# Kernel optimization log

Measured on AMD Instinct MI355X. Metric: run time of the kernel, lower is better.

Reference implementation:

```python
import jax, jax.numpy as jnp
import numpy as np

B, T, EMB, HEAD = 8, 4096, 1024, 64  # batch, seq (=block_sz), emb_dim, head_sz


def setup_inputs() -> dict:
    key = jax.random.key(0)
    kx, kw = jax.random.split(key)
    x = jax.random.normal(kx, (B, T, EMB), dtype=jnp.float32)
    W = jax.random.normal(kw, (EMB, 3 * HEAD), dtype=jnp.float32) * 0.02
    return {"x": x, "W": W}


def reference(x, W):
    # fused QKV projection: [B,T,EMB] @ [EMB,3*HEAD] -> [B,T,3*HEAD]
    kqv = x @ W
    k, q, v = jnp.split(kqv, 3, axis=-1)  # source order: k, q, v
    head_sz = q.shape[-1]
    # causal attention scores: [B,T,T]
    scores = jnp.einsum('btd,bsd->bts', q, k) / jnp.sqrt(jnp.float32(head_sz))
    causal_mask = jnp.triu(jnp.full((scores.shape[1], scores.shape[2]), -jnp.inf, dtype=scores.dtype), 1)
    w = jax.nn.softmax(scores + causal_mask, axis=-1)
    # dropout p=0.0 -> identity
    out = jnp.einsum('bts,bsd->btd', w, v)  # [B,T,HEAD]
    return out
```

## Files before the change

kernel.cpp:

```cpp
#include <hip/hip_runtime.h>
#include <hip/hip_bf16.h>

#define BATCH 8
#define SEQ 4096
#define EMB 1024
#define HEAD 64
#define N3 192

#define BM 64
#define BK 64
#define NT (EMB / BK)
#define LSTR 72

typedef __attribute__((ext_vector_type(4))) float f32x4;
typedef __attribute__((ext_vector_type(8))) short bf16x8;
typedef __attribute__((ext_vector_type(4))) short short4v;
typedef __attribute__((ext_vector_type(4))) float float4v;
typedef __attribute__((ext_vector_type(2))) unsigned int u32x2;

#define LOG2E 1.4426950408889634f
#define QSCALE (0.125f * LOG2E)


static __device__ __forceinline__ unsigned short f2bf(float f) {
  unsigned int x = __builtin_bit_cast(unsigned int, f);
  x += 0x7fffu + ((x >> 16) & 1u);
  return (unsigned short)(x >> 16);
}

__global__ __launch_bounds__(256) void wt_kernel(const float* __restrict__ W,
                                                 unsigned short* __restrict__ Wt) {
  int idx = blockIdx.x * 256 + threadIdx.x;
  int k = idx / N3, c = idx % N3;
  Wt[(size_t)c * EMB + k] = f2bf(W[idx]);
}

__global__ __launch_bounds__(256, 2) void qkv_kernel(const float* __restrict__ x,
                                                     const unsigned short* __restrict__ Wt,
                                                     unsigned short* __restrict__ PK,
                                                     unsigned short* __restrict__ PQ,
                                                     unsigned short* __restrict__ PV) {
  __shared__ unsigned short Asm[2][BM][LSTR];
  __shared__ unsigned short Bsm[2][N3][LSTR];

  const int tid = threadIdx.x;
  const int wid = tid >> 6;
  const int lane = tid & 63;
  const int l16 = lane & 15;
  const int lg = lane >> 4;
  const int m0 = blockIdx.x * BM;

  const int ar0 = tid >> 4;
  const int ac4 = tid & 15;
  const int br0 = tid >> 3;
  const int bc = tid & 7;

  const float* xa = x + (size_t)(m0 + ar0) * EMB + ac4 * 4;
  const unsigned short* wb = Wt + (size_t)br0 * EMB + bc * 8;

  f32x4 acc[4][3];
#pragma unroll
  for (int mi = 0; mi < 4; ++mi)
#pragma unroll
    for (int ni = 0; ni < 3; ++ni) acc[mi][ni] = (f32x4)0.0f;

  float4v av[4];
  bf16x8 bv[6];

#define ISSUE_LOADS(K0)                                                        \
  {                                                                            \
    _Pragma("unroll") for (int i = 0; i < 4; ++i)                              \
        av[i] = *(const float4v*)(xa + (size_t)(16 * i) * EMB + (K0));         \
    _Pragma("unroll") for (int i = 0; i < 6; ++i)                              \
        bv[i] = *(const bf16x8*)(wb + (size_t)(32 * i) * EMB + (K0));          \
  }

#define WRITE_LDS(BUF)                                                         \
  {                                                                            \
    _Pragma("unroll") for (int i = 0; i < 4; ++i) {                            \
      short4v p;                                                               \
      _Pragma("unroll") for (int j = 0; j < 4; ++j)                            \
          p[j] = (short)f2bf(av[i][j]);                                        \
      *(short4v*)&Asm[BUF][ar0 + 16 * i][ac4 * 4] = p;                         \
    }                                                                          \
    _Pragma("unroll") for (int i = 0; i < 6; ++i)                              \
        *(bf16x8*)&Bsm[BUF][br0 + 32 * i][bc * 8] = bv[i];                     \
  }

#define COMPUTE(BUF)                                                           \
  {                                                                            \
    _Pragma("unroll") for (int kh = 0; kh < 2; ++kh) {                         \
      bf16x8 af[4], bfr[3];                                                    \
      _Pragma("unroll") for (int mi = 0; mi < 4; ++mi)                         \
          af[mi] = *(const bf16x8*)&Asm[BUF][mi * 16 + l16][kh * 32 + lg * 8]; \
      _Pragma("unroll") for (int ni = 0; ni < 3; ++ni)                         \
          bfr[ni] = *(const bf16x8*)&Bsm[BUF][wid * 48 + ni * 16 + l16][kh * 32 + lg * 8]; \
      _Pragma("unroll") for (int mi = 0; mi < 4; ++mi)                         \
        _Pragma("unroll") for (int ni = 0; ni < 3; ++ni)                       \
            acc[mi][ni] = __builtin_amdgcn_mfma_f32_16x16x32_bf16(             \
                af[mi], bfr[ni], acc[mi][ni], 0, 0, 0);                        \
    }                                                                          \
  }

  ISSUE_LOADS(0)
  WRITE_LDS(0)
  __syncthreads();

  int cur = 0;
  for (int t = 0; t < NT; ++t) {
    if (t < NT - 1) ISSUE_LOADS((t + 1) * BK)
    COMPUTE(cur)
    if (t < NT - 1) {
      WRITE_LDS(cur ^ 1)
    }
    __syncthreads();
    cur ^= 1;
  }
#undef ISSUE_LOADS
#undef WRITE_LDS
#undef COMPUTE

#pragma unroll
  for (int mi = 0; mi < 4; ++mi) {
#pragma unroll
    for (int ni = 0; ni < 3; ++ni) {
      const int n = wid * 48 + ni * 16 + l16;
#pragma unroll
      for (int r = 0; r < 4; ++r) {
        const int row = m0 + mi * 16 + lg * 4 + r;
        const int bb = row >> 12;
        const int ss = row & (SEQ - 1);
        const float v = acc[mi][ni][r];
        if (n < 64) {
          PK[(((size_t)bb * 256 + (ss >> 4)) * 2 + (n >> 5)) * 512 +
             (ss & 15) * 32 + (n & 31)] = f2bf(v);
        } else if (n < 128) {
          const int d = n - 64;
          PQ[(((size_t)bb * 256 + (ss >> 4)) * 2 + (d >> 5)) * 512 +
             (ss & 15) * 32 + (d & 31)] = f2bf(v * QSCALE);
        } else {
          const int d = n - 128;
          PV[(((size_t)bb * 64 + (ss >> 6)) * 8 + (d >> 4) * 2 + ((ss >> 5) & 1)) * 512 +
             (d & 15) * 32 + (ss & 31)] = f2bf(v);
        }
      }
    }
  }
}

__global__ __launch_bounds__(256, 4) void attn_kernel(const unsigned short* __restrict__ PK,
                                                      const unsigned short* __restrict__ PQ,
                                                      const unsigned short* __restrict__ PV,
                                                      float* __restrict__ out) {
  __shared__ float Msm[4][16];
  __shared__ float Lsm[4][16];
  __shared__ float Osm[4][4][16][17];
  __shared__ unsigned short Pl[4][2][16][LSTR];

  const int tid = threadIdx.x;
  const int wid = tid >> 6;
  const int lane = tid & 63;
  const int l16 = lane & 15;
  const int lg = lane >> 4;
  const int lam = (l16 * 4 + lg) * 8;

  const int Bid = blockIdx.x;
  const int b = Bid & 7;
  const int i_ = (Bid >> 3) & 31;
  const int j_ = Bid >> 8;
  const int p = (j_ == 0) ? i_ : (j_ == 1) ? (127 - i_) : (j_ == 2) ? (32 + i_) : (95 - i_);
  const int qc0 = 2 * p, qc1 = 2 * p + 1;
  const int q0a = qc0 * 16, q0b = qc1 * 16;
  const int T_total = (q0b + 16 + 63) >> 6;
  const int t0 = (wid * T_total) >> 2;
  const int t1 = ((wid + 1) * T_total) >> 2;

  const unsigned short* pkb = PK + (size_t)b * 256 * 1024;
  const unsigned short* pqb = PQ + (size_t)b * 256 * 1024;
  const unsigned short* pvb = PV + (size_t)b * 64 * 8 * 512;

  bf16x8 qa0 = *(const bf16x8*)(pqb + ((size_t)qc0 * 2 + 0) * 512 + lam);
  bf16x8 qa1 = *(const bf16x8*)(pqb + ((size_t)qc0 * 2 + 1) * 512 + lam);
  bf16x8 qb0 = *(const bf16x8*)(pqb + ((size_t)qc1 * 2 + 0) * 512 + lam);
  bf16x8 qb1 = *(const bf16x8*)(pqb + ((size_t)qc1 * 2 + 1) * 512 + lam);

  f32x4 oA[4], oB[4];
#pragma unroll
  for (int dd = 0; dd < 4; ++dd) { oA[dd] = (f32x4)0.0f; oB[dd] = (f32x4)0.0f; }
  float mA = -3.0e38f, lA = 0.0f, mB = -3.0e38f, lB = 0.0f;

  for (int it = t0; it < t1; ++it) {
    const int kv0 = it << 6;

    f32x4 s0[4], s1[4];
#pragma unroll
    for (int t = 0; t < 4; ++t) {
      const unsigned short* kp = pkb + ((size_t)(it * 4 + t) * 2) * 512 + lam;
      bf16x8 kfa = *(const bf16x8*)(kp);
      bf16x8 kfb = *(const bf16x8*)(kp + 512);
      f32x4 z = (f32x4)0.0f;
      z = __builtin_amdgcn_mfma_f32_16x16x32_bf16(kfa, qa0, z, 0, 0, 0);
      s0[t] = __builtin_amdgcn_mfma_f32_16x16x32_bf16(kfb, qa1, z, 0, 0, 0);
      z = (f32x4)0.0f;
      z = __builtin_amdgcn_mfma_f32_16x16x32_bf16(kfa, qb0, z, 0, 0, 0);
      s1[t] = __builtin_amdgcn_mfma_f32_16x16x32_bf16(kfb, qb1, z, 0, 0, 0);
    }

    bf16x8 vf[8];
#pragma unroll
    for (int dd = 0; dd < 4; ++dd) {
      const unsigned short* vp = pvb + ((size_t)it * 8 + dd * 2) * 512 + lam;
      vf[2 * dd] = *(const bf16x8*)(vp);
      vf[2 * dd + 1] = *(const bf16x8*)(vp + 512);
    }

    if (kv0 + 64 > q0a) {
      const int base = kv0 + lg * 4 - q0a - l16;
#pragma unroll
      for (int t = 0; t < 4; ++t)
#pragma unroll
        for (int r = 0; r < 4; ++r)
          if (base + 16 * t + r > 0) s0[t][r] = -3.0e38f;
    }
    {
      float mx = s0[0][0];
#pragma unroll
      for (int t = 0; t < 4; ++t)
#pragma unroll
        for (int r = 0; r < 4; ++r) mx = fmaxf(mx, s0[t][r]);
      mx = fmaxf(mx, __shfl_xor(mx, 16));
      mx = fmaxf(mx, __shfl_xor(mx, 32));
      if (!__all(mx <= mA)) {
        float mn = fmaxf(mA, mx);
        float al = exp2f(mA - mn);
        mA = mn; lA *= al;
#pragma unroll
        for (int dd = 0; dd < 4; ++dd) oA[dd] *= al;
      }
      float ps = 0.0f;
#pragma unroll
      for (int t = 0; t < 4; ++t) {
        float p0 = exp2f(s0[t][0] - mA);
        float p1 = exp2f(s0[t][1] - mA);
        float p2 = exp2f(s0[t][2] - mA);
        float p3 = exp2f(s0[t][3] - mA);
        ps += (p0 + p1) + (p2 + p3);
        u32x2 w;
        w[0] = (__builtin_bit_cast(unsigned int, p1) & 0xFFFF0000u) |
               (__builtin_bit_cast(unsigned int, p0) >> 16);
        w[1] = (__builtin_bit_cast(unsigned int, p3) & 0xFFFF0000u) |
               (__builtin_bit_cast(unsigned int, p2) >> 16);
        *(u32x2*)&Pl[wid][0][l16][16 * t + lg * 4] = w;
      }
      ps += __shfl_xor(ps, 16);
      ps += __shfl_xor(ps, 32);
      lA += ps;
    }
    {
      bf16x8 pf0 = *(const bf16x8*)&Pl[wid][0][l16][lg * 8];
      bf16x8 pf1 = *(const bf16x8*)&Pl[wid][0][l16][32 + lg * 8];
#pragma unroll
      for (int dd = 0; dd < 4; ++dd) {
        oA[dd] = __builtin_amdgcn_mfma_f32_16x16x32_bf16(vf[2 * dd], pf0, oA[dd], 0, 0, 0);
        oA[dd] = __builtin_amdgcn_mfma_f32_16x16x32_bf16(vf[2 * dd + 1], pf1, oA[dd], 0, 0, 0);
      }
    }

    if (kv0 + 64 > q0b) {
      const int base = kv0 + lg * 4 - q0b - l16;
#pragma unroll
      for (int t = 0; t < 4; ++t)
#pragma unroll
        for (int r = 0; r < 4; ++r)
          if (base + 16 * t + r > 0) s1[t][r] = -3.0e38f;
    }
    {
      float mx = s1[0][0];
#pragma unroll
      for (int t = 0; t < 4; ++t)
#pragma unroll
        for (int r = 0; r < 4; ++r) mx = fmaxf(mx, s1[t][r]);
      mx = fmaxf(mx, __shfl_xor(mx, 16));
      mx = fmaxf(mx, __shfl_xor(mx, 32));
      if (!__all(mx <= mB)) {
        float mn = fmaxf(mB, mx);
        float al = exp2f(mB - mn);
        mB = mn; lB *= al;
#pragma unroll
        for (int dd = 0; dd < 4; ++dd) oB[dd] *= al;
      }
      float ps = 0.0f;
#pragma unroll
      for (int t = 0; t < 4; ++t) {
        float p0 = exp2f(s1[t][0] - mB);
        float p1 = exp2f(s1[t][1] - mB);
        float p2 = exp2f(s1[t][2] - mB);
        float p3 = exp2f(s1[t][3] - mB);
        ps += (p0 + p1) + (p2 + p3);
        u32x2 w;
        w[0] = (__builtin_bit_cast(unsigned int, p1) & 0xFFFF0000u) |
               (__builtin_bit_cast(unsigned int, p0) >> 16);
        w[1] = (__builtin_bit_cast(unsigned int, p3) & 0xFFFF0000u) |
               (__builtin_bit_cast(unsigned int, p2) >> 16);
        *(u32x2*)&Pl[wid][1][l16][16 * t + lg * 4] = w;
      }
      ps += __shfl_xor(ps, 16);
      ps += __shfl_xor(ps, 32);
      lB += ps;
    }
    {
      bf16x8 pf0 = *(const bf16x8*)&Pl[wid][1][l16][lg * 8];
      bf16x8 pf1 = *(const bf16x8*)&Pl[wid][1][l16][32 + lg * 8];
#pragma unroll
      for (int dd = 0; dd < 4; ++dd) {
        oB[dd] = __builtin_amdgcn_mfma_f32_16x16x32_bf16(vf[2 * dd], pf0, oB[dd], 0, 0, 0);
        oB[dd] = __builtin_amdgcn_mfma_f32_16x16x32_bf16(vf[2 * dd + 1], pf1, oB[dd], 0, 0, 0);
      }
    }
  }

#define MERGE_PHASE(MV, LV, OV, Q0)                                            \
  {                                                                            \
    if (lg == 0) { Msm[wid][l16] = MV; Lsm[wid][l16] = LV; }                   \
    _Pragma("unroll") for (int dd = 0; dd < 4; ++dd)                           \
      _Pragma("unroll") for (int r = 0; r < 4; ++r)                            \
          Osm[wid][dd][lg * 4 + r][l16] = OV[dd][r];                           \
    __syncthreads();                                                           \
    if (wid == 0) {                                                            \
      float M = Msm[0][l16];                                                   \
      _Pragma("unroll") for (int w = 1; w < 4; ++w) M = fmaxf(M, Msm[w][l16]); \
      float L = 0.0f;                                                          \
      f32x4 oc[4];                                                             \
      _Pragma("unroll") for (int dd = 0; dd < 4; ++dd) oc[dd] = (f32x4)0.0f;   \
      _Pragma("unroll") for (int w = 0; w < 4; ++w) {                          \
        float sc = exp2f(Msm[w][l16] - M);                                     \
        L += Lsm[w][l16] * sc;                                                 \
        _Pragma("unroll") for (int dd = 0; dd < 4; ++dd)                       \
          _Pragma("unroll") for (int r = 0; r < 4; ++r)                        \
              oc[dd][r] += Osm[w][dd][lg * 4 + r][l16] * sc;                   \
      }                                                                        \
      const float inv = 1.0f / L;                                              \
      float* op = out + ((size_t)b * SEQ + (Q0) + l16) * HEAD;                 \
      _Pragma("unroll") for (int dd = 0; dd < 4; ++dd)                         \
        _Pragma("unroll") for (int r = 0; r < 4; ++r)                          \
            op[16 * dd + lg * 4 + r] = oc[dd][r] * inv;                        \
    }                                                                          \
    __syncthreads();                                                           \
  }
  MERGE_PHASE(mA, lA, oA, q0a)
  MERGE_PHASE(mB, lB, oB, q0b)
#undef MERGE_PHASE
}

extern "C" void kernel_launch(void* const* d_in, const int* in_sizes, int n_in,
                              void* d_out, int out_size, void* d_ws, size_t ws_size,
                              hipStream_t stream) {
  (void)in_sizes; (void)n_in; (void)out_size; (void)ws_size;
  const float* x = (const float*)d_in[0];
  const float* W = (const float*)d_in[1];
  float* out = (float*)d_out;

  const size_t MB4 = (size_t)4 * 1024 * 1024;
  unsigned short* Wt = (unsigned short*)d_ws;
  unsigned short* PK = (unsigned short*)((char*)d_ws + 512 * 1024);
  unsigned short* PQ = (unsigned short*)((char*)d_ws + 512 * 1024 + MB4);
  unsigned short* PV = (unsigned short*)((char*)d_ws + 512 * 1024 + 2 * MB4);

  hipLaunchKernelGGL(wt_kernel, dim3((EMB * N3) / 256), dim3(256), 0, stream, W, Wt);
  hipLaunchKernelGGL(qkv_kernel, dim3((BATCH * SEQ) / BM), dim3(256), 0, stream, x, Wt, PK, PQ, PV);
  hipLaunchKernelGGL(attn_kernel, dim3(BATCH * 128), dim3(256), 0, stream, PK, PQ, PV, out);
}
```

Measured before the change: 101.8 us.

## Software-pipeline K tile loads, raise MFMA priority, relax launch bounds

Prefetches the next iteration's K fragments into registers (double-buffered kf/kn) so global load latency overlaps with the current tile's compute. It also wraps the MFMA sections in s_setprio to favour matrix instructions across waves. Launch bounds drop from 4 to 3 blocks per SM to give the extra live registers room. The prefetch reads one tile past t1 on the last iteration, which may touch memory beyond the batch slice or the buffer, and lower occupancy could reduce latency hiding.

Result: faster. 86.36 us (-15.2%).

```diff
diff --git a/kernel.cpp b/kernel.cpp
--- a/kernel.cpp
+++ b/kernel.cpp
@@ -148,7 +148,7 @@
   }
 }
 
-__global__ __launch_bounds__(256, 4) void attn_kernel(const unsigned short* __restrict__ PK,
+__global__ __launch_bounds__(256, 3) void attn_kernel(const unsigned short* __restrict__ PK,
                                                       const unsigned short* __restrict__ PQ,
                                                       const unsigned short* __restrict__ PV,
                                                       float* __restrict__ out) {
@@ -175,9 +175,7 @@
   const int t0 = (wid * T_total) >> 2;
   const int t1 = ((wid + 1) * T_total) >> 2;
 
-  const unsigned short* pkb = PK + (size_t)b * 256 * 1024;
   const unsigned short* pqb = PQ + (size_t)b * 256 * 1024;
-  const unsigned short* pvb = PV + (size_t)b * 64 * 8 * 512;
 
   bf16x8 qa0 = *(const bf16x8*)(pqb + ((size_t)qc0 * 2 + 0) * 512 + lam);
   bf16x8 qa1 = *(const bf16x8*)(pqb + ((size_t)qc0 * 2 + 1) * 512 + lam);
@@ -189,133 +187,157 @@
   for (int dd = 0; dd < 4; ++dd) { oA[dd] = (f32x4)0.0f; oB[dd] = (f32x4)0.0f; }
   float mA = -3.0e38f, lA = 0.0f, mB = -3.0e38f, lB = 0.0f;
 
-  for (int it = t0; it < t1; ++it) {
-    const int kv0 = it << 6;
-
-    f32x4 s0[4], s1[4];
+  const unsigned short* kp = PK + (size_t)b * 256 * 1024 + (size_t)t0 * 4096 + lam;
+  const unsigned short* vp = PV + (size_t)b * 64 * 8 * 512 + (size_t)t0 * 4096 + lam;
+
+  if (t0 < t1) {
+    bf16x8 kf[8], kn[8];
 #pragma unroll
     for (int t = 0; t < 4; ++t) {
-      const unsigned short* kp = pkb + ((size_t)(it * 4 + t) * 2) * 512 + lam;
-      bf16x8 kfa = *(const bf16x8*)(kp);
-      bf16x8 kfb = *(const bf16x8*)(kp + 512);
-      f32x4 z = (f32x4)0.0f;
-      z = __builtin_amdgcn_mfma_f32_16x16x32_bf16(kfa, qa0, z, 0, 0, 0);
-      s0[t] = __builtin_amdgcn_mfma_f32_16x16x32_bf16(kfb, qa1, z, 0, 0, 0);
-      z = (f32x4)0.0f;
-      z = __builtin_amdgcn_mfma_f32_16x16x32_bf16(kfa, qb0, z, 0, 0, 0);
-      s1[t] = __builtin_amdgcn_mfma_f32_16x16x32_bf16(kfb, qb1, z, 0, 0, 0);
+      kf[2 * t] = *(const bf16x8*)(kp + t * 1024);
+      kf[2 * t + 1] = *(const bf16x8*)(kp + t * 1024 + 512);
     }
 
-    bf16x8 vf[8];
-#pragma unroll
-    for (int dd = 0; dd < 4; ++dd) {
-      const unsigned short* vp = pvb + ((size_t)it * 8 + dd * 2) * 512 + lam;
-      vf[2 * dd] = *(const bf16x8*)(vp);
-      vf[2 * dd + 1] = *(const bf16x8*)(vp + 512);
-    }
-
-    if (kv0 + 64 > q0a) {
-      const int base = kv0 + lg * 4 - q0a - l16;
-#pragma unroll
-      for (int t = 0; t < 4; ++t)
-#pragma unroll
-        for (int r = 0; r < 4; ++r)
-          if (base + 16 * t + r > 0) s0[t][r] = -3.0e38f;
-    }
-    {
-      float mx = s0[0][0];
-#pragma unroll
-      for (int t = 0; t < 4; ++t)
-#pragma unroll
-        for (int r = 0; r < 4; ++r) mx = fmaxf(mx, s0[t][r]);
-      mx = fmaxf(mx, __shfl_xor(mx, 16));
-      mx = fmaxf(mx, __shfl_xor(mx, 32));
-      if (!__all(mx <= mA)) {
-        float mn = fmaxf(mA, mx);
-        float al = exp2f(mA - mn);
-        mA = mn; lA *= al;
-#pragma unroll
-        for (int dd = 0; dd < 4; ++dd) oA[dd] *= al;
-      }
-      float ps = 0.0f;
+    for (int it = t0; it < t1; ++it) {
+      const int kv0 = it << 6;
+
 #pragma unroll
       for (int t = 0; t < 4; ++t) {
-        float p0 = exp2f(s0[t][0] - mA);
-        float p1 = exp2f(s0[t][1] - mA);
-        float p2 = exp2f(s0[t][2] - mA);
-        float p3 = exp2f(s0[t][3] - mA);
-        ps += (p0 + p1) + (p2 + p3);
-        u32x2 w;
-        w[0] = (__builtin_bit_cast(unsigned int, p1) & 0xFFFF0000u) |
-               (__builtin_bit_cast(unsigned int, p0) >> 16);
-        w[1] = (__builtin_bit_cast(unsigned int, p3) & 0xFFFF0000u) |
-               (__builtin_bit_cast(unsigned int, p2) >> 16);
-        *(u32x2*)&Pl[wid][0][l16][16 * t + lg * 4] = w;
-      }
-      ps += __shfl_xor(ps, 16);
-      ps += __shfl_xor(ps, 32);
-      lA += ps;
-    }
-    {
-      bf16x8 pf0 = *(const bf16x8*)&Pl[wid][0][l16][lg * 8];
-      bf16x8 pf1 = *(const bf16x8*)&Pl[wid][0][l16][32 + lg * 8];
+        kn[2 * t] = *(const bf16x8*)(kp + 4096 + t * 1024);
+        kn[2 * t + 1] = *(const bf16x8*)(kp + 4096 + t * 1024 + 512);
+      }
+      bf16x8 vf[8];
 #pragma unroll
       for (int dd = 0; dd < 4; ++dd) {
-        oA[dd] = __builtin_amdgcn_mfma_f32_16x16x32_bf16(vf[2 * dd], pf0, oA[dd], 0, 0, 0);
-        oA[dd] = __builtin_amdgcn_mfma_f32_16x16x32_bf16(vf[2 * dd + 1], pf1, oA[dd], 0, 0, 0);
-      }
-    }
-
-    if (kv0 + 64 > q0b) {
-      const int base = kv0 + lg * 4 - q0b - l16;
-#pragma unroll
-      for (int t = 0; t < 4; ++t)
-#pragma unroll
-        for (int r = 0; r < 4; ++r)
-          if (base + 16 * t + r > 0) s1[t][r] = -3.0e38f;
-    }
-    {
-      float mx = s1[0][0];
-#pragma unroll
-      for (int t = 0; t < 4; ++t)
-#pragma unroll
-        for (int r = 0; r < 4; ++r) mx = fmaxf(mx, s1[t][r]);
-      mx = fmaxf(mx, __shfl_xor(mx, 16));
-      mx = fmaxf(mx, __shfl_xor(mx, 32));
-      if (!__all(mx <= mB)) {
-        float mn = fmaxf(mB, mx);
-        float al = exp2f(mB - mn);
-        mB = mn; lB *= al;
-#pragma unroll
-        for (int dd = 0; dd < 4; ++dd) oB[dd] *= al;
-      }
-      float ps = 0.0f;
+        vf[2 * dd] = *(const bf16x8*)(vp + dd * 1024);
+        vf[2 * dd + 1] = *(const bf16x8*)(vp + dd * 1024 + 512);
+      }
+
+      f32x4 s0[4], s1[4];
+      __builtin_amdgcn_s_setprio(1);
 #pragma unroll
       for (int t = 0; t < 4; ++t) {
-        float p0 = exp2f(s1[t][0] - mB);
-        float p1 = exp2f(s1[t][1] - mB);
-        float p2 = exp2f(s1[t][2] - mB);
-        float p3 = exp2f(s1[t][3] - mB);
-        ps += (p0 + p1) + (p2 + p3);
-        u32x2 w;
-        w[0] = (__builtin_bit_cast(unsigned int, p1) & 0xFFFF0000u) |
-               (__builtin_bit_cast(unsigned int, p0) >> 16);
-        w[1] = (__builtin_bit_cast(unsigned int, p3) & 0xFFFF0000u) |
-               (__builtin_bit_cast(unsigned int, p2) >> 16);
-        *(u32x2*)&Pl[wid][1][l16][16 * t + lg * 4] = w;
-      }
-      ps += __shfl_xor(ps, 16);
-      ps += __shfl_xor(ps, 32);
-      lB += ps;
-    }
-    {
-      bf16x8 pf0 = *(const bf16x8*)&Pl[wid][1][l16][lg * 8];
-      bf16x8 pf1 = *(const bf16x8*)&Pl[wid][1][l16][32 + lg * 8];
-#pragma unroll
-      for (int dd = 0; dd < 4; ++dd) {
-        oB[dd] = __builtin_amdgcn_mfma_f32_16x16x32_bf16(vf[2 * dd], pf0, oB[dd], 0, 0, 0);
-        oB[dd] = __builtin_amdgcn_mfma_f32_16x16x32_bf16(vf[2 * dd + 1], pf1, oB[dd], 0, 0, 0);
-      }
+        f32x4 z = (f32x4)0.0f;
+        z = __builtin_amdgcn_mfma_f32_16x16x32_bf16(kf[2 * t], qa0, z, 0, 0, 0);
+        s0[t] = __builtin_amdgcn_mfma_f32_16x16x32_bf16(kf[2 * t + 1], qa1, z, 0, 0, 0);
+        z = (f32x4)0.0f;
+        z = __builtin_amdgcn_mfma_f32_16x16x32_bf16(kf[2 * t], qb0, z, 0, 0, 0);
+        s1[t] = __builtin_amdgcn_mfma_f32_16x16x32_bf16(kf[2 * t + 1], qb1, z, 0, 0, 0);
+      }
+      __builtin_amdgcn_s_setprio(0);
+
+      if (kv0 + 64 > q0a) {
+        const int base = kv0 + lg * 4 - q0a - l16;
+#pragma unroll
+        for (int t = 0; t < 4; ++t)
+#pragma unroll
+          for (int r = 0; r < 4; ++r)
+            if (base + 16 * t + r > 0) s0[t][r] = -3.0e38f;
+      }
+      {
+        float mx = s0[0][0];
+#pragma unroll
+        for (int t = 0; t < 4; ++t)
+#pragma unroll
+          for (int r = 0; r < 4; ++r) mx = fmaxf(mx, s0[t][r]);
+        mx = fmaxf(mx, __shfl_xor(mx, 16));
+        mx = fmaxf(mx, __shfl_xor(mx, 32));
+        if (!__all(mx <= mA)) {
+          float mn = fmaxf(mA, mx);
+          float al = exp2f(mA - mn);
+          mA = mn; lA *= al;
+#pragma unroll
+          for (int dd = 0; dd < 4; ++dd) oA[dd] *= al;
+        }
+        float ps = 0.0f;
+#pragma unroll
+        for (int t = 0; t < 4; ++t) {
+          float p0 = exp2f(s0[t][0] - mA);
+          float p1 = exp2f(s0[t][1] - mA);
+          float p2 = exp2f(s0[t][2] - mA);
+          float p3 = exp2f(s0[t][3] - mA);
+          ps += (p0 + p1) + (p2 + p3);
+          u32x2 w;
+          w[0] = (__builtin_bit_cast(unsigned int, p1) & 0xFFFF0000u) |
+                 (__builtin_bit_cast(unsigned int, p0) >> 16);
+          w[1] = (__builtin_bit_cast(unsigned int, p3) & 0xFFFF0000u) |
+                 (__builtin_bit_cast(unsigned int, p2) >> 16);
+          *(u32x2*)&Pl[wid][0][l16][16 * t + lg * 4] = w;
+        }
+        ps += __shfl_xor(ps, 16);
+        ps += __shfl_xor(ps, 32);
+        lA += ps;
+      }
+      {
+        bf16x8 pf0 = *(const bf16x8*)&Pl[wid][0][l16][lg * 8];
+        bf16x8 pf1 = *(const bf16x8*)&Pl[wid][0][l16][32 + lg * 8];
+        __builtin_amdgcn_s_setprio(1);
+#pragma unroll
+        for (int dd = 0; dd < 4; ++dd) {
+          oA[dd] = __builtin_amdgcn_mfma_f32_16x16x32_bf16(vf[2 * dd], pf0, oA[dd], 0, 0, 0);
+          oA[dd] = __builtin_amdgcn_mfma_f32_16x16x32_bf16(vf[2 * dd + 1], pf1, oA[dd], 0, 0, 0);
+        }
+        __builtin_amdgcn_s_setprio(0);
+      }
+
+      if (kv0 + 64 > q0b) {
+        const int base = kv0 + lg * 4 - q0b - l16;
+#pragma unroll
+        for (int t = 0; t < 4; ++t)
+#pragma unroll
+          for (int r = 0; r < 4; ++r)
+            if (base + 16 * t + r > 0) s1[t][r] = -3.0e38f;
+      }
+      {
+        float mx = s1[0][0];
+#pragma unroll
+        for (int t = 0; t < 4; ++t)
+#pragma unroll
+          for (int r = 0; r < 4; ++r) mx = fmaxf(mx, s1[t][r]);
+        mx = fmaxf(mx, __shfl_xor(mx, 16));
+        mx = fmaxf(mx, __shfl_xor(mx, 32));
+        if (!__all(mx <= mB)) {
+          float mn = fmaxf(mB, mx);
+          float al = exp2f(mB - mn);
+          mB = mn; lB *= al;
+#pragma unroll
+          for (int dd = 0; dd < 4; ++dd) oB[dd] *= al;
+        }
+        float ps = 0.0f;
+#pragma unroll
+        for (int t = 0; t < 4; ++t) {
+          float p0 = exp2f(s1[t][0] - mB);
+          float p1 = exp2f(s1[t][1] - mB);
+          float p2 = exp2f(s1[t][2] - mB);
+          float p3 = exp2f(s1[t][3] - mB);
+          ps += (p0 + p1) + (p2 + p3);
+          u32x2 w;
+          w[0] = (__builtin_bit_cast(unsigned int, p1) & 0xFFFF0000u) |
+                 (__builtin_bit_cast(unsigned int, p0) >> 16);
+          w[1] = (__builtin_bit_cast(unsigned int, p3) & 0xFFFF0000u) |
+                 (__builtin_bit_cast(unsigned int, p2) >> 16);
+          *(u32x2*)&Pl[wid][1][l16][16 * t + lg * 4] = w;
+        }
+        ps += __shfl_xor(ps, 16);
+        ps += __shfl_xor(ps, 32);
+        lB += ps;
+      }
+      {
+        bf16x8 pf0 = *(const bf16x8*)&Pl[wid][1][l16][lg * 8];
+        bf16x8 pf1 = *(const bf16x8*)&Pl[wid][1][l16][32 + lg * 8];
+        __builtin_amdgcn_s_setprio(1);
+#pragma unroll
+        for (int dd = 0; dd < 4; ++dd) {
+          oB[dd] = __builtin_amdgcn_mfma_f32_16x16x32_bf16(vf[2 * dd], pf0, oB[dd], 0, 0, 0);
+          oB[dd] = __builtin_amdgcn_mfma_f32_16x16x32_bf16(vf[2 * dd + 1], pf1, oB[dd], 0, 0, 0);
+        }
+        __builtin_amdgcn_s_setprio(0);
+      }
+
+#pragma unroll
+      for (int j = 0; j < 8; ++j) kf[j] = kn[j];
+      kp += 4096;
+      vp += 4096;
     }
   }
 
```
